# Optimization experiments

Hardware: AMD Instinct MI355X
Metric: run time of the kernel (lower is better)

Reference implementation:

```python
import jax, jax.numpy as jnp
import numpy as np
from jax import lax

N, T, IN, H, HEADS, OUT, E = 20000, 32, 32, 64, 4, 1, 320000


def setup_inputs() -> dict:
    key = jax.random.key(0)
    ks = jax.random.split(key, 18)
    s = 0.1
    inp = {
        "x": jax.random.normal(ks[0], (N, T, IN), jnp.float32),
        "edge_index": jax.random.randint(ks[1], (2, E), 0, N, dtype=jnp.int32),
        # LSTM layer 0 (PyTorch gate order i,f,g,o)
        "l0_Wih": jax.random.normal(ks[2], (4 * H, IN), jnp.float32) * s,
        "l0_Whh": jax.random.normal(ks[3], (4 * H, H), jnp.float32) * s,
        "l0_bih": jax.random.normal(ks[4], (4 * H,), jnp.float32) * s,
        "l0_bhh": jax.random.normal(ks[5], (4 * H,), jnp.float32) * s,
        # LSTM layer 1
        "l1_Wih": jax.random.normal(ks[6], (4 * H, H), jnp.float32) * s,
        "l1_Whh": jax.random.normal(ks[7], (4 * H, H), jnp.float32) * s,
        "l1_bih": jax.random.normal(ks[8], (4 * H,), jnp.float32) * s,
        "l1_bhh": jax.random.normal(ks[9], (4 * H,), jnp.float32) * s,
        # GAT layer 1: in=H, out=H, heads=HEADS (concat)
        "g1_w": jax.random.normal(ks[10], (H, HEADS * H), jnp.float32) * s,
        "g1_as": jax.random.normal(ks[11], (1, HEADS, H), jnp.float32) * s,
        "g1_ad": jax.random.normal(ks[12], (1, HEADS, H), jnp.float32) * s,
        "g1_b": jnp.zeros((HEADS * H,), jnp.float32),
        # GAT layer 2: in=HEADS*H, out=OUT, heads=1
        "g2_w": jax.random.normal(ks[13], (HEADS * H, OUT), jnp.float32) * s,
        "g2_as": jax.random.normal(ks[14], (1, 1, OUT), jnp.float32) * s,
        "g2_ad": jax.random.normal(ks[15], (1, 1, OUT), jnp.float32) * s,
        "g2_b": jnp.zeros((OUT,), jnp.float32),
    }
    return inp


def _lstm_layer(x, Wih, Whh, bih, bhh):
    # x: [N, T, F] -> [N, T, H]
    n = x.shape[0]
    h0 = jnp.zeros((n, Whh.shape[1]), x.dtype)

    def step(carry, xt):
        h, c = carry
        g = xt @ Wih.T + h @ Whh.T + bih + bhh  # [N, 4H]
        i, f, gg, o = jnp.split(g, 4, axis=-1)
        c = jax.nn.sigmoid(f) * c + jax.nn.sigmoid(i) * jnp.tanh(gg)
        h = jax.nn.sigmoid(o) * jnp.tanh(c)
        return (h, c), h

    _, hs = lax.scan(step, (h0, h0), jnp.swapaxes(x, 0, 1))
    return jnp.swapaxes(hs, 0, 1)


def _gat(x, src, dst, n, W, a_src, a_dst, b, heads, outc):
    # PyG GATConv (eval mode, add_self_loops already applied to src/dst)
    xh = (x @ W).reshape(n, heads, outc)              # [N, heads, C]
    al_s = (xh * a_src).sum(-1)                       # [N, heads]
    al_d = (xh * a_dst).sum(-1)
    e = jax.nn.leaky_relu(al_s[src] + al_d[dst], 0.2)  # [E, heads]
    m = jax.ops.segment_max(e, dst, num_segments=n)
    m = jnp.where(jnp.isfinite(m), m, 0.0)
    ex = jnp.exp(e - m[dst])
    den = jax.ops.segment_sum(ex, dst, num_segments=n)
    w = ex / (den[dst] + 1e-16)                       # segment softmax over dst
    out = jax.ops.segment_sum(xh[src] * w[..., None], dst, num_segments=n)
    return out.reshape(n, heads * outc) + b


def reference(x, edge_index, l0_Wih, l0_Whh, l0_bih, l0_bhh, l1_Wih, l1_Whh,
              l1_bih, l1_bhh, g1_w, g1_as, g1_ad, g1_b, g2_w, g2_as, g2_ad, g2_b):
    n = x.shape[0]
    loops = jnp.arange(n, dtype=edge_index.dtype)
    ei = jnp.concatenate([edge_index, jnp.stack([loops, loops])], axis=1)
    src, dst = ei[0], ei[1]
    h = _lstm_layer(x, l0_Wih, l0_Whh, l0_bih, l0_bhh)
    h = _lstm_layer(h, l1_Wih, l1_Whh, l1_bih, l1_bhh)
    h = h[:, -1, :]  # node features from last timestep
    h = jax.nn.relu(_gat(h, src, dst, n, g1_w, g1_as, g1_ad, g1_b, HEADS, H))
    return _gat(h, src, dst, n, g2_w, g2_as, g2_ad, g2_b, 1, OUT)
```

## Files before the change

### kernel.cpp

```cpp
#include <hip/hip_runtime.h>
#include <math.h>

#define NN   20000
#define TT   32
#define INF_ 32
#define HID  64
#define NH   4
#define EE   320000
#define ETOT (EE + NN)
#define ZROW 164
#define NB   80

typedef __attribute__((ext_vector_type(8))) short bf16x8;
typedef __attribute__((ext_vector_type(4))) short short4v;
typedef __attribute__((ext_vector_type(4))) float f32x4;

static __device__ __forceinline__ float lrelu(float x){ return x>0.0f ? x : 0.2f*x; }

static __device__ __forceinline__ unsigned short f2bf(float f){
  unsigned u = __float_as_uint(f);
  unsigned r = u + 0x7fffu + ((u>>16)&1u);
  return (unsigned short)(r>>16);
}
static __device__ __forceinline__ float bf2f(unsigned short h){ return __uint_as_float(((unsigned)h)<<16); }

static __device__ __forceinline__ float lstm_cell(float gi, float gf, float gg, float go, float& c){
  float ef = __expf(-gf), ei = __expf(-gi), eg = __expf(-2.0f*gg);
  float pN = c*(1.0f+ei)*(1.0f+eg) + (1.0f-eg)*(1.0f+ef);
  float pD = (1.0f+ef)*(1.0f+ei)*(1.0f+eg);
  float cc = pN * __builtin_amdgcn_rcpf(pD);
  c = cc;
  float eo = __expf(-go), ec = __expf(-2.0f*cc);
  return (1.0f-ec) * __builtin_amdgcn_rcpf((1.0f+eo)*(1.0f+ec));
}

static __device__ __forceinline__ void edge_sd(const int* __restrict__ ei, int e, int& s, int& d){
  if (e < EE){ s = ei[e]; d = ei[EE + e]; } else { s = e - EE; d = s; }
}

__global__ void kzero_int(int* __restrict__ p, int n){
  int i = blockIdx.x*256 + threadIdx.x;
  if (i < n) p[i] = 0;
}

__global__ void pack_weights(const float* __restrict__ Wih0, const float* __restrict__ Whh0,
                             const float* __restrict__ bih0, const float* __restrict__ bhh0,
                             const float* __restrict__ Wih1, const float* __restrict__ Whh1,
                             const float* __restrict__ bih1, const float* __restrict__ bhh1,
                             unsigned short* __restrict__ Wpk,
                             float* __restrict__ b0, float* __restrict__ b1){
  int idx = blockIdx.x*256 + threadIdx.x;
  if (idx < 49152){
    int fb = idx >> 9;
    int h  = fb & 1;
    int t2 = fb >> 1;
    int ks = t2 % 3, tl = t2 / 3;
    int r  = idx & 511;
    int l  = r >> 3, j = r & 7;
    int pr = l & 15;
    int g  = (pr&3)*64 + tl*4 + (pr>>2);
    int k  = ks*32 + 4*(l>>4) + (j & 3) + 16*(j >> 2);
    float src = (k < 32) ? Wih0[g*32 + k] : Whh0[g*64 + (k - 32)];
    unsigned short hi = f2bf(src);
    Wpk[idx] = h ? f2bf(src - bf2f(hi)) : hi;
  } else if (idx < 114688){
    int idx2 = idx - 49152;
    int fb = idx2 >> 9;
    int h  = fb & 1;
    int t2 = fb >> 1;
    int ks = t2 & 3, tl = t2 >> 2;
    int r  = idx2 & 511;
    int l  = r >> 3, j = r & 7;
    int pr = l & 15;
    int g  = (pr&3)*64 + tl*4 + (pr>>2);
    int k  = ks*32 + 4*(l>>4) + (j & 3) + 16*(j >> 2);
    float src = (k < 64) ? Wih1[g*64 + k] : Whh1[g*64 + (k - 64)];
    unsigned short hi = f2bf(src);
    Wpk[idx] = h ? f2bf(src - bf2f(hi)) : hi;
  } else {
    int m = idx - 114688;
    if (m < 256) b0[m] = bih0[m] + bhh0[m];
    else if (m < 512) b1[m-256] = bih1[m-256] + bhh1[m-256];
  }
}

__global__ void count_deg(const int* __restrict__ ei, int* __restrict__ deg){
  int e = blockIdx.x*256 + threadIdx.x;
  if (e >= ETOT) return;
  int s, d; edge_sd(ei, e, s, d);
  atomicAdd(deg + d, 1);
}

__global__ void scan_deg(const int* __restrict__ deg, int* __restrict__ indptr, int* __restrict__ cursor){
  __shared__ int part[256];
  const int t = threadIdx.x;
  const int CH = (NN + 255) / 256;
  const int c0 = t * CH;
  int sum = 0;
  for (int i=0;i<CH;i++){ int idx=c0+i; if (idx<NN) sum += deg[idx]; }
  part[t] = sum; __syncthreads();
  int val = sum;
  for (int off=1; off<256; off<<=1){
    int add = (t>=off) ? part[t-off] : 0;
    __syncthreads();
    val += add; part[t] = val;
    __syncthreads();
  }
  int run = val - sum;
  for (int i=0;i<CH;i++){
    int idx=c0+i;
    if (idx<NN){ indptr[idx]=run; cursor[idx]=run; run += deg[idx]; }
  }
  if (t == 0) indptr[NN] = ETOT;
}

__global__ void scatter_edges(const int* __restrict__ ei, int* __restrict__ cursor, int* __restrict__ csr_src){
  int e = blockIdx.x*256 + threadIdx.x;
  if (e >= ETOT) return;
  int s, d; edge_sd(ei, e, s, d);
  int pos = atomicAdd(cursor + d, 1);
  csr_src[pos] = s;
}

#define PIN_LOAD(dst, p) asm volatile( \
    "global_load_dwordx4 %0, %1, off\n\t" \
    "s_waitcnt vmcnt(0)" \
    : "=&v"(dst) : "v"(p))

__global__ __launch_bounds__(1024)
__attribute__((amdgpu_waves_per_eu(4, 4)))
void lstm_mfma(
    const float* __restrict__ x,
    const unsigned short* __restrict__ Wpk,
    const float* __restrict__ b0, const float* __restrict__ b1,
    float* __restrict__ h1out)
{
  __shared__ unsigned short Zh[NB*ZROW];
  __shared__ unsigned short Zl[NB*ZROW];

  const int tid  = threadIdx.x;
  const int lane = tid & 63;
  const int w    = __builtin_amdgcn_readfirstlane(tid >> 6);
  const int ln15 = lane & 15;
  const int lq   = lane >> 4;
  const int gbase = blockIdx.x * NB;

  const bf16x8* wp = (const bf16x8*)Wpk;

  bf16x8 wA0h[3], wA0l[3], wA1h[4], wA1l[4];
#pragma unroll
  for (int ks=0; ks<3; ++ks){
    PIN_LOAD(wA0h[ks], wp + ((w*3+ks)*2+0)*64 + lane);
    PIN_LOAD(wA0l[ks], wp + ((w*3+ks)*2+1)*64 + lane);
  }
#pragma unroll
  for (int ks=0; ks<4; ++ks){
    PIN_LOAD(wA1h[ks], wp + 6144 + ((w*4+ks)*2+0)*64 + lane);
    PIN_LOAD(wA1l[ks], wp + 6144 + ((w*4+ks)*2+1)*64 + lane);
  }

  f32x4 bv0, bv1;
  {
    const int u = w*4 + lq;
#pragma unroll
    for (int j=0; j<4; ++j){ bv0[j] = b0[j*64+u]; bv1[j] = b1[j*64+u]; }
  }

  const int xn = tid >> 3;
  const int xk = (tid & 7) * 4;
  const float* xp = x + (size_t)(gbase + ((xn < NB) ? xn : 0))*(TT*INF_) + xk;
  const bool xth = (tid < 640);

  for (int i = tid; i < NB*ZROW/2; i += 1024){ ((unsigned*)Zh)[i] = 0; ((unsigned*)Zl)[i] = 0; }
  __syncthreads();
  if (xth){
    float4 v = *(const float4*)xp;
    unsigned short h_[4], l_[4];
    h_[0]=f2bf(v.x); h_[1]=f2bf(v.y); h_[2]=f2bf(v.z); h_[3]=f2bf(v.w);
    l_[0]=f2bf(v.x-bf2f(h_[0])); l_[1]=f2bf(v.y-bf2f(h_[1]));
    l_[2]=f2bf(v.z-bf2f(h_[2])); l_[3]=f2bf(v.w-bf2f(h_[3]));
    *(uint2*)&Zh[xn*ZROW + xk] = make_uint2((unsigned)h_[0]|((unsigned)h_[1]<<16),(unsigned)h_[2]|((unsigned)h_[3]<<16));
    *(uint2*)&Zl[xn*ZROW + xk] = make_uint2((unsigned)l_[0]|((unsigned)l_[1]<<16),(unsigned)l_[2]|((unsigned)l_[3]<<16));
  }
  __syncthreads();

  float c0[5], c1[5];
#pragma unroll
  for (int i=0;i<5;i++){ c0[i]=0.f; c1[i]=0.f; }
  f32x4 aL1[5];

#define ZFRAG(Zb, node, kz) ({                                            \
    const unsigned short* _p = &Zb[(node)*ZROW + (kz) + 4*lq];            \
    short4v _a = *(const short4v*)_p;                                     \
    short4v _b = *(const short4v*)(_p + 16);                              \
    __builtin_shufflevector(_a, _b, 0,1,2,3,4,5,6,7); })

#define MF(acc, A, B) acc = __builtin_amdgcn_mfma_f32_16x16x32_bf16((A),(B),(acc),0,0,0)

#define HWRITE(hv, col) {                                                 \
    const unsigned short _hh = f2bf(hv);                                  \
    Zh[_n*ZROW + (col)] = _hh;                                            \
    Zl[_n*ZROW + (col)] = f2bf((hv) - bf2f(_hh)); }

  for (int t=0; t<TT; ++t){
    float4 xv;
    const bool dox = xth && (t+1 < TT);
    if (dox) xv = *(const float4*)(xp + (size_t)(t+1)*INF_);

    if (t > 0){
      const int uc = 96 + w*4 + lq;
#pragma unroll
      for (int GG=0; GG<5; ++GG){
        const int _n = GG*16 + ln15;
        float h = lstm_cell(aL1[GG][0], aL1[GG][1], aL1[GG][2], aL1[GG][3], c1[GG]);
        HWRITE(h, uc);
      }
    }

    f32x4 aL0[5];
#pragma unroll
    for (int GG=0; GG<5; ++GG) aL0[GG] = bv0;

#pragma unroll
    for (int ks=0; ks<3; ++ks){
      const int kz = ks*32;
#pragma unroll
      for (int GG=0; GG<5; ++GG){
        const bf16x8 zh = ZFRAG(Zh, GG*16+ln15, kz);
        const bf16x8 zl = ZFRAG(Zl, GG*16+ln15, kz);
        MF(aL0[GG], wA0h[ks], zh); MF(aL0[GG], wA0h[ks], zl); MF(aL0[GG], wA0l[ks], zh);
      }
    }
    __syncthreads();

    {
      const int uc = 32 + w*4 + lq;
#pragma unroll
      for (int GG=0; GG<5; ++GG){
        const int _n = GG*16 + ln15;
        float h = lstm_cell(aL0[GG][0], aL0[GG][1], aL0[GG][2], aL0[GG][3], c0[GG]);
        HWRITE(h, uc);
      }
    }
    if (dox){
      unsigned short h_[4], l_[4];
      h_[0]=f2bf(xv.x); h_[1]=f2bf(xv.y); h_[2]=f2bf(xv.z); h_[3]=f2bf(xv.w);
      l_[0]=f2bf(xv.x-bf2f(h_[0])); l_[1]=f2bf(xv.y-bf2f(h_[1]));
      l_[2]=f2bf(xv.z-bf2f(h_[2])); l_[3]=f2bf(xv.w-bf2f(h_[3]));
      *(uint2*)&Zh[xn*ZROW + xk] = make_uint2((unsigned)h_[0]|((unsigned)h_[1]<<16),(unsigned)h_[2]|((unsigned)h_[3]<<16));
      *(uint2*)&Zl[xn*ZROW + xk] = make_uint2((unsigned)l_[0]|((unsigned)l_[1]<<16),(unsigned)l_[2]|((unsigned)l_[3]<<16));
    }

#pragma unroll
    for (int GG=0; GG<5; ++GG) aL1[GG] = bv1;

#pragma unroll
    for (int ks=2; ks<4; ++ks){
      const int kz = 32 + ks*32;
#pragma unroll
      for (int GG=0; GG<5; ++GG){
        const bf16x8 zh = ZFRAG(Zh, GG*16+ln15, kz);
        const bf16x8 zl = ZFRAG(Zl, GG*16+ln15, kz);
        MF(aL1[GG], wA1h[ks], zh); MF(aL1[GG], wA1h[ks], zl); MF(aL1[GG], wA1l[ks], zh);
      }
    }
    __syncthreads();

#pragma unroll
    for (int ks=0; ks<2; ++ks){
      const int kz = 32 + ks*32;
#pragma unroll
      for (int GG=0; GG<5; ++GG){
        const bf16x8 zh = ZFRAG(Zh, GG*16+ln15, kz);
        const bf16x8 zl = ZFRAG(Zl, GG*16+ln15, kz);
        MF(aL1[GG], wA1h[ks], zh); MF(aL1[GG], wA1h[ks], zl); MF(aL1[GG], wA1l[ks], zh);
      }
    }
    __syncthreads();
  }

  {
    const int uc = 96 + w*4 + lq;
#pragma unroll
    for (int GG=0; GG<5; ++GG){
      const int _n = GG*16 + ln15;
      float h = lstm_cell(aL1[GG][0], aL1[GG][1], aL1[GG][2], aL1[GG][3], c1[GG]);
      HWRITE(h, uc);
    }
  }
  __syncthreads();

  for (int o = tid; o < NB*64; o += 1024){
    const int n = o >> 6, u = o & 63;
    h1out[(size_t)(gbase+n)*64 + u] = bf2f(Zh[n*ZROW + 96 + u]) + bf2f(Zl[n*ZROW + 96 + u]);
  }
#undef ZFRAG
#undef MF
#undef HWRITE
}

__global__ __launch_bounds__(256) void gat1_prep(const float* __restrict__ h1, const float* __restrict__ W,
  const float* __restrict__ as_, const float* __restrict__ ad_,
  float* __restrict__ xh, float* __restrict__ als, float* __restrict__ ald)
{
  __shared__ float hs[8][64];
  const int nb0 = blockIdx.x * 8;
  const int o  = threadIdx.x;
  const int q  = o >> 6, u = o & 63;
  for (int i = o; i < 512; i += 256){
    hs[i>>6][i&63] = h1[(size_t)(nb0 + (i>>6))*64 + (i&63)];
  }
  __syncthreads();
  float acc[8];
#pragma unroll
  for (int nd=0; nd<8; ++nd) acc[nd] = 0.f;
  for (int k=0; k<64; ++k){
    const float wv = W[k*256 + o];
#pragma unroll
    for (int nd=0; nd<8; ++nd) acc[nd] = fmaf(hs[nd][k], wv, acc[nd]);
  }
  const float asv = as_[o], adv = ad_[o];
#pragma unroll
  for (int nd=0; nd<8; ++nd){
    xh[(size_t)(nb0+nd)*256 + o] = acc[nd];
    float ps = acc[nd] * asv;
    float pd = acc[nd] * adv;
#pragma unroll
    for (int off=32; off>=1; off>>=1){ ps += __shfl_xor(ps, off); pd += __shfl_xor(pd, off); }
    if (u == 0){ als[(nb0+nd)*4 + q] = ps; ald[(nb0+nd)*4 + q] = pd; }
  }
}

__global__ __launch_bounds__(256) void gat1_gather(
  const int* __restrict__ indptr, const int* __restrict__ csr_src,
  const float* __restrict__ als, const float* __restrict__ ald,
  const float* __restrict__ xh,  const float* __restrict__ b1g,
  const float* __restrict__ w2,  const float* __restrict__ as2, const float* __restrict__ ad2,
  float* __restrict__ xh2, float* __restrict__ a2s, float* __restrict__ a2d)
{
  const int d = blockIdx.x*4 + (threadIdx.x >> 6);
  const int lane = threadIdx.x & 63;
  if (d >= NN) return;
  const int p0 = indptr[d], p1 = indptr[d+1];

  float aldv[4];
#pragma unroll
  for (int q=0;q<4;q++) aldv[q] = ald[d*4+q];

  float mx[4];
#pragma unroll
  for (int q=0;q<4;q++) mx[q] = -3.4e38f;
  for (int e=p0+lane; e<p1; e+=64){
    int s = csr_src[e];
#pragma unroll
    for (int q=0;q<4;q++){
      float ev = lrelu(als[s*4+q] + aldv[q]);
      mx[q] = fmaxf(mx[q], ev);
    }
  }
#pragma unroll
  for (int off=32; off>=1; off>>=1){
#pragma unroll
    for (int q=0;q<4;q++) mx[q] = fmaxf(mx[q], __shfl_xor(mx[q], off));
  }

  const int q = lane >> 4;
  const float mq = mx[q];
  const float aldq = aldv[q];
  float ax=0.f, ay=0.f, az=0.f, aw=0.f, den=0.f;
  int s_next = (p0 < p1) ? csr_src[p0] : 0;
  for (int e=p0; e<p1; ++e){
    const int s = s_next;
    if (e+1 < p1) s_next = csr_src[e+1];
    float ev = lrelu(als[s*4+q] + aldq);
    float ex = __expf(ev - mq);
    den += ex;
    float4 v = *(const float4*)(xh + (size_t)s*256 + lane*4);
    ax = fmaf(ex, v.x, ax); ay = fmaf(ex, v.y, ay);
    az = fmaf(ex, v.z, az); aw = fmaf(ex, v.w, aw);
  }
  const float rr = 1.0f/(den + 1e-16f);
  const int o = lane*4;
  float v0 = ax*rr + b1g[o+0];
  float v1 = ay*rr + b1g[o+1];
  float v2 = az*rr + b1g[o+2];
  float v3 = aw*rr + b1g[o+3];
  v0 = v0>0.f?v0:0.f; v1 = v1>0.f?v1:0.f; v2 = v2>0.f?v2:0.f; v3 = v3>0.f?v3:0.f;
  float part = v0*w2[o+0] + v1*w2[o+1] + v2*w2[o+2] + v3*w2[o+3];
#pragma unroll
  for (int off=32; off>=1; off>>=1) part += __shfl_xor(part, off);
  if (lane == 0){
    xh2[d] = part;
    a2s[d] = part * as2[0];
    a2d[d] = part * ad2[0];
  }
}

__global__ __launch_bounds__(256) void gat2_gather(
  const int* __restrict__ indptr, const int* __restrict__ csr_src,
  const float* __restrict__ a2s, const float* __restrict__ a2d,
  const float* __restrict__ xh2, const float* __restrict__ b2,
  float* __restrict__ out)
{
  const int d = blockIdx.x*4 + (threadIdx.x >> 6);
  const int lane = threadIdx.x & 63;
  if (d >= NN) return;
  const int p0 = indptr[d], p1 = indptr[d+1];
  const float add = a2d[d];

  float mx = -3.4e38f;
  for (int e=p0+lane; e<p1; e+=64){
    int s = csr_src[e];
    mx = fmaxf(mx, lrelu(a2s[s] + add));
  }
#pragma unroll
  for (int off=32; off>=1; off>>=1) mx = fmaxf(mx, __shfl_xor(mx, off));

  float den = 0.f, num = 0.f;
  for (int e=p0+lane; e<p1; e+=64){
    int s = csr_src[e];
    float ev = lrelu(a2s[s] + add);
    float ex = __expf(ev - mx);
    den += ex;
    num = fmaf(ex, xh2[s], num);
  }
#pragma unroll
  for (int off=32; off>=1; off>>=1){ den += __shfl_xor(den, off); num += __shfl_xor(num, off); }
  if (lane == 0) out[d] = num/(den + 1e-16f) + b2[0];
}

extern "C" void kernel_launch(void* const* d_in, const int* in_sizes, int n_in,
                              void* d_out, int out_size, void* d_ws, size_t ws_size,
                              hipStream_t stream)
{
  const float* x    = (const float*)d_in[0];
  const int*   ei   = (const int*)d_in[1];
  const float* Wih0 = (const float*)d_in[2];
  const float* Whh0 = (const float*)d_in[3];
  const float* bih0 = (const float*)d_in[4];
  const float* bhh0 = (const float*)d_in[5];
  const float* Wih1 = (const float*)d_in[6];
  const float* Whh1 = (const float*)d_in[7];
  const float* bih1 = (const float*)d_in[8];
  const float* bhh1 = (const float*)d_in[9];
  const float* g1w  = (const float*)d_in[10];
  const float* g1as = (const float*)d_in[11];
  const float* g1ad = (const float*)d_in[12];
  const float* g1b  = (const float*)d_in[13];
  const float* g2w  = (const float*)d_in[14];
  const float* g2as = (const float*)d_in[15];
  const float* g2ad = (const float*)d_in[16];
  const float* g2b  = (const float*)d_in[17];

  float* ws  = (float*)d_ws;
  unsigned short* Wpk = (unsigned short*)ws;
  float* b0  = ws + 57344;
  float* b1  = b0 + 256;
  float* h1  = b1 + 256;
  float* xh  = h1 + 1280000;
  float* als = xh + 5120000;
  float* ald = als + 80000;
  float* xh2 = ald + 80000;
  float* a2s = xh2 + 20000;
  float* a2d = a2s + 20000;
  int*   deg    = (int*)(a2d + 20000);
  int*   indptr = deg + 20000;
  int*   cursor = indptr + 20001;
  int*   csr    = cursor + 20000;

  kzero_int<<<(NN+255)/256, 256, 0, stream>>>(deg, NN);
  pack_weights<<<450, 256, 0, stream>>>(Wih0,Whh0,bih0,bhh0,Wih1,Whh1,bih1,bhh1,Wpk,b0,b1);
  count_deg<<<(ETOT+255)/256, 256, 0, stream>>>(ei, deg);
  scan_deg<<<1, 256, 0, stream>>>(deg, indptr, cursor);
  scatter_edges<<<(ETOT+255)/256, 256, 0, stream>>>(ei, cursor, csr);
  lstm_mfma<<<250, 1024, 0, stream>>>(x, Wpk, b0, b1, h1);
  gat1_prep<<<NN/8, 256, 0, stream>>>(h1, g1w, g1as, g1ad, xh, als, ald);
  gat1_gather<<<(NN+3)/4, 256, 0, stream>>>(indptr, csr, als, ald, xh, g1b, g2w, g2as, g2ad, xh2, a2s, a2d);
  gat2_gather<<<(NN+3)/4, 256, 0, stream>>>(indptr, csr, a2s, a2d, xh2, g2b, (float*)d_out);
}
```

Baseline: 412.9 us.

## Reschedule LSTM MFMA chunks around barriers, pack bf16 conversions, widen GAT prep tile

Reorders the fused two-layer LSTM time loop so MFMA chunks that do not depend on freshly written hidden state are interleaved with the gate nonlinearities. This removes one __syncthreads per timestep by carrying the final layer-1 chunks across the loop boundary. The fp32-to-bf16 hi/lo splitting now uses the packed v_cvt_pk_bf16_f32 instruction to cut ALU work. gat1_prep processes 16 nodes per block instead of 8 to reuse each weight load more. The barrier reordering depends on subtle LDS read/write ordering, and the larger accumulator raises register pressure.

```diff
diff --git a/kernel.cpp b/kernel.cpp
--- a/kernel.cpp
+++ b/kernel.cpp
@@ -171,16 +171,24 @@
   const float* xp = x + (size_t)(gbase + ((xn < NB) ? xn : 0))*(TT*INF_) + xk;
   const bool xth = (tid < 640);
 
+#define XSTAGE(v) {                                                       \
+    unsigned pkA, pkB, plA, plB;                                          \
+    asm("v_cvt_pk_bf16_f32 %0,%1,%2":"=v"(pkA):"v"((v).x),"v"((v).y));    \
+    asm("v_cvt_pk_bf16_f32 %0,%1,%2":"=v"(pkB):"v"((v).z),"v"((v).w));    \
+    float l0_ = (v).x - __uint_as_float(pkA<<16);                         \
+    float l1_ = (v).y - __uint_as_float(pkA & 0xffff0000u);               \
+    float l2_ = (v).z - __uint_as_float(pkB<<16);                         \
+    float l3_ = (v).w - __uint_as_float(pkB & 0xffff0000u);               \
+    asm("v_cvt_pk_bf16_f32 %0,%1,%2":"=v"(plA):"v"(l0_),"v"(l1_));        \
+    asm("v_cvt_pk_bf16_f32 %0,%1,%2":"=v"(plB):"v"(l2_),"v"(l3_));        \
+    *(uint2*)&Zh[xn*ZROW + xk] = make_uint2(pkA, pkB);                    \
+    *(uint2*)&Zl[xn*ZROW + xk] = make_uint2(plA, plB); }
+
   for (int i = tid; i < NB*ZROW/2; i += 1024){ ((unsigned*)Zh)[i] = 0; ((unsigned*)Zl)[i] = 0; }
   __syncthreads();
   if (xth){
     float4 v = *(const float4*)xp;
-    unsigned short h_[4], l_[4];
-    h_[0]=f2bf(v.x); h_[1]=f2bf(v.y); h_[2]=f2bf(v.z); h_[3]=f2bf(v.w);
-    l_[0]=f2bf(v.x-bf2f(h_[0])); l_[1]=f2bf(v.y-bf2f(h_[1]));
-    l_[2]=f2bf(v.z-bf2f(h_[2])); l_[3]=f2bf(v.w-bf2f(h_[3]));
-    *(uint2*)&Zh[xn*ZROW + xk] = make_uint2((unsigned)h_[0]|((unsigned)h_[1]<<16),(unsigned)h_[2]|((unsigned)h_[3]<<16));
-    *(uint2*)&Zl[xn*ZROW + xk] = make_uint2((unsigned)l_[0]|((unsigned)l_[1]<<16),(unsigned)l_[2]|((unsigned)l_[3]<<16));
+    XSTAGE(v);
   }
   __syncthreads();
 
@@ -197,96 +205,87 @@
 
 #define MF(acc, A, B) acc = __builtin_amdgcn_mfma_f32_16x16x32_bf16((A),(B),(acc),0,0,0)
 
-#define HWRITE(hv, col) {                                                 \
+#define WPAIR(ha, hb, GA, GB, col) {                                      \
+    unsigned pk_, pl_;                                                    \
+    asm("v_cvt_pk_bf16_f32 %0,%1,%2":"=v"(pk_):"v"(ha),"v"(hb));          \
+    float la_ = (ha) - __uint_as_float(pk_<<16);                          \
+    float lb_ = (hb) - __uint_as_float(pk_ & 0xffff0000u);                \
+    asm("v_cvt_pk_bf16_f32 %0,%1,%2":"=v"(pl_):"v"(la_),"v"(lb_));        \
+    Zh[((GA)*16+ln15)*ZROW + (col)] = (unsigned short)pk_;                \
+    Zh[((GB)*16+ln15)*ZROW + (col)] = (unsigned short)(pk_>>16);          \
+    Zl[((GA)*16+ln15)*ZROW + (col)] = (unsigned short)pl_;                \
+    Zl[((GB)*16+ln15)*ZROW + (col)] = (unsigned short)(pl_>>16); }
+
+#define WSINGLE(hv, GG, col) {                                            \
+    const int _n = (GG)*16 + ln15;                                        \
     const unsigned short _hh = f2bf(hv);                                  \
     Zh[_n*ZROW + (col)] = _hh;                                            \
     Zl[_n*ZROW + (col)] = f2bf((hv) - bf2f(_hh)); }
+
+#define CHUNK(ACCS, KZ, WH, WL)                                           \
+    _Pragma("unroll")                                                     \
+    for (int GG=0; GG<5; ++GG){                                           \
+      const bf16x8 zh = ZFRAG(Zh, GG*16+ln15, KZ);                        \
+      const bf16x8 zl = ZFRAG(Zl, GG*16+ln15, KZ);                        \
+      MF(ACCS[GG], WH, zh); MF(ACCS[GG], WH, zl); MF(ACCS[GG], WL, zh);   \
+    }
 
   for (int t=0; t<TT; ++t){
     float4 xv;
     const bool dox = xth && (t+1 < TT);
     if (dox) xv = *(const float4*)(xp + (size_t)(t+1)*INF_);
 
+    f32x4 aL0[5];
+#pragma unroll
+    for (int GG=0; GG<5; ++GG) aL0[GG] = bv0;
+
+    CHUNK(aL0, 0, wA0h[0], wA0l[0]);
+
     if (t > 0){
       const int uc = 96 + w*4 + lq;
-#pragma unroll
-      for (int GG=0; GG<5; ++GG){
-        const int _n = GG*16 + ln15;
-        float h = lstm_cell(aL1[GG][0], aL1[GG][1], aL1[GG][2], aL1[GG][3], c1[GG]);
-        HWRITE(h, uc);
-      }
+      float h0_ = lstm_cell(aL1[0][0], aL1[0][1], aL1[0][2], aL1[0][3], c1[0]);
+      float h1_ = lstm_cell(aL1[1][0], aL1[1][1], aL1[1][2], aL1[1][3], c1[1]);
+      float h2_ = lstm_cell(aL1[2][0], aL1[2][1], aL1[2][2], aL1[2][3], c1[2]);
+      float h3_ = lstm_cell(aL1[3][0], aL1[3][1], aL1[3][2], aL1[3][3], c1[3]);
+      float h4_ = lstm_cell(aL1[4][0], aL1[4][1], aL1[4][2], aL1[4][3], c1[4]);
+      WPAIR(h0_, h1_, 0, 1, uc); WPAIR(h2_, h3_, 2, 3, uc); WSINGLE(h4_, 4, uc);
     }
 
-    f32x4 aL0[5];
-#pragma unroll
-    for (int GG=0; GG<5; ++GG) aL0[GG] = bv0;
-
-#pragma unroll
-    for (int ks=0; ks<3; ++ks){
-      const int kz = ks*32;
-#pragma unroll
-      for (int GG=0; GG<5; ++GG){
-        const bf16x8 zh = ZFRAG(Zh, GG*16+ln15, kz);
-        const bf16x8 zl = ZFRAG(Zl, GG*16+ln15, kz);
-        MF(aL0[GG], wA0h[ks], zh); MF(aL0[GG], wA0h[ks], zl); MF(aL0[GG], wA0l[ks], zh);
-      }
-    }
+    CHUNK(aL0, 32, wA0h[1], wA0l[1]);
+    CHUNK(aL0, 64, wA0h[2], wA0l[2]);
     __syncthreads();
+
+#pragma unroll
+    for (int GG=0; GG<5; ++GG) aL1[GG] = bv1;
+
+    CHUNK(aL1, 96, wA1h[2], wA1l[2]);
 
     {
       const int uc = 32 + w*4 + lq;
-#pragma unroll
-      for (int GG=0; GG<5; ++GG){
-        const int _n = GG*16 + ln15;
-        float h = lstm_cell(aL0[GG][0], aL0[GG][1], aL0[GG][2], aL0[GG][3], c0[GG]);
-        HWRITE(h, uc);
-      }
+      float h0_ = lstm_cell(aL0[0][0], aL0[0][1], aL0[0][2], aL0[0][3], c0[0]);
+      float h1_ = lstm_cell(aL0[1][0], aL0[1][1], aL0[1][2], aL0[1][3], c0[1]);
+      float h2_ = lstm_cell(aL0[2][0], aL0[2][1], aL0[2][2], aL0[2][3], c0[2]);
+      float h3_ = lstm_cell(aL0[3][0], aL0[3][1], aL0[3][2], aL0[3][3], c0[3]);
+      float h4_ = lstm_cell(aL0[4][0], aL0[4][1], aL0[4][2], aL0[4][3], c0[4]);
+      WPAIR(h0_, h1_, 0, 1, uc); WPAIR(h2_, h3_, 2, 3, uc); WSINGLE(h4_, 4, uc);
     }
-    if (dox){
-      unsigned short h_[4], l_[4];
-      h_[0]=f2bf(xv.x); h_[1]=f2bf(xv.y); h_[2]=f2bf(xv.z); h_[3]=f2bf(xv.w);
-      l_[0]=f2bf(xv.x-bf2f(h_[0])); l_[1]=f2bf(xv.y-bf2f(h_[1]));
-      l_[2]=f2bf(xv.z-bf2f(h_[2])); l_[3]=f2bf(xv.w-bf2f(h_[3]));
-      *(uint2*)&Zh[xn*ZROW + xk] = make_uint2((unsigned)h_[0]|((unsigned)h_[1]<<16),(unsigned)h_[2]|((unsigned)h_[3]<<16));
-      *(uint2*)&Zl[xn*ZROW + xk] = make_uint2((unsigned)l_[0]|((unsigned)l_[1]<<16),(unsigned)l_[2]|((unsigned)l_[3]<<16));
-    }
-
-#pragma unroll
-    for (int GG=0; GG<5; ++GG) aL1[GG] = bv1;
-
-#pragma unroll
-    for (int ks=2; ks<4; ++ks){
-      const int kz = 32 + ks*32;
-#pragma unroll
-      for (int GG=0; GG<5; ++GG){
-        const bf16x8 zh = ZFRAG(Zh, GG*16+ln15, kz);
-        const bf16x8 zl = ZFRAG(Zl, GG*16+ln15, kz);
-        MF(aL1[GG], wA1h[ks], zh); MF(aL1[GG], wA1h[ks], zl); MF(aL1[GG], wA1l[ks], zh);
-      }
-    }
+    if (dox) XSTAGE(xv);
+
+    CHUNK(aL1, 128, wA1h[3], wA1l[3]);
     __syncthreads();
 
-#pragma unroll
-    for (int ks=0; ks<2; ++ks){
-      const int kz = 32 + ks*32;
-#pragma unroll
-      for (int GG=0; GG<5; ++GG){
-        const bf16x8 zh = ZFRAG(Zh, GG*16+ln15, kz);
-        const bf16x8 zl = ZFRAG(Zl, GG*16+ln15, kz);
-        MF(aL1[GG], wA1h[ks], zh); MF(aL1[GG], wA1h[ks], zl); MF(aL1[GG], wA1l[ks], zh);
-      }
-    }
-    __syncthreads();
+    CHUNK(aL1, 32, wA1h[0], wA1l[0]);
+    CHUNK(aL1, 64, wA1h[1], wA1l[1]);
   }
 
   {
     const int uc = 96 + w*4 + lq;
-#pragma unroll
-    for (int GG=0; GG<5; ++GG){
-      const int _n = GG*16 + ln15;
-      float h = lstm_cell(aL1[GG][0], aL1[GG][1], aL1[GG][2], aL1[GG][3], c1[GG]);
-      HWRITE(h, uc);
-    }
+    float h0_ = lstm_cell(aL1[0][0], aL1[0][1], aL1[0][2], aL1[0][3], c1[0]);
+    float h1_ = lstm_cell(aL1[1][0], aL1[1][1], aL1[1][2], aL1[1][3], c1[1]);
+    float h2_ = lstm_cell(aL1[2][0], aL1[2][1], aL1[2][2], aL1[2][3], c1[2]);
+    float h3_ = lstm_cell(aL1[3][0], aL1[3][1], aL1[3][2], aL1[3][3], c1[3]);
+    float h4_ = lstm_cell(aL1[4][0], aL1[4][1], aL1[4][2], aL1[4][3], c1[4]);
+    WPAIR(h0_, h1_, 0, 1, uc); WPAIR(h2_, h3_, 2, 3, uc); WSINGLE(h4_, 4, uc);
   }
   __syncthreads();
 
@@ -296,32 +295,35 @@
   }
 #undef ZFRAG
 #undef MF
-#undef HWRITE
+#undef WPAIR
+#undef WSINGLE
+#undef CHUNK
+#undef XSTAGE
 }
 
 __global__ __launch_bounds__(256) void gat1_prep(const float* __restrict__ h1, const float* __restrict__ W,
   const float* __restrict__ as_, const float* __restrict__ ad_,
   float* __restrict__ xh, float* __restrict__ als, float* __restrict__ ald)
 {
-  __shared__ float hs[8][64];
-  const int nb0 = blockIdx.x * 8;
+  __shared__ float hs[16][64];
+  const int nb0 = blockIdx.x * 16;
   const int o  = threadIdx.x;
   const int q  = o >> 6, u = o & 63;
-  for (int i = o; i < 512; i += 256){
+  for (int i = o; i < 1024; i += 256){
     hs[i>>6][i&63] = h1[(size_t)(nb0 + (i>>6))*64 + (i&63)];
   }
   __syncthreads();
-  float acc[8];
-#pragma unroll
-  for (int nd=0; nd<8; ++nd) acc[nd] = 0.f;
+  float acc[16];
+#pragma unroll
+  for (int nd=0; nd<16; ++nd) acc[nd] = 0.f;
   for (int k=0; k<64; ++k){
     const float wv = W[k*256 + o];
 #pragma unroll
-    for (int nd=0; nd<8; ++nd) acc[nd] = fmaf(hs[nd][k], wv, acc[nd]);
+    for (int nd=0; nd<16; ++nd) acc[nd] = fmaf(hs[nd][k], wv, acc[nd]);
   }
   const float asv = as_[o], adv = ad_[o];
 #pragma unroll
-  for (int nd=0; nd<8; ++nd){
+  for (int nd=0; nd<16; ++nd){
     xh[(size_t)(nb0+nd)*256 + o] = acc[nd];
     float ps = acc[nd] * asv;
     float pd = acc[nd] * adv;
@@ -474,7 +476,7 @@
   scan_deg<<<1, 256, 0, stream>>>(deg, indptr, cursor);
   scatter_edges<<<(ETOT+255)/256, 256, 0, stream>>>(ei, cursor, csr);
   lstm_mfma<<<250, 1024, 0, stream>>>(x, Wpk, b0, b1, h1);
-  gat1_prep<<<NN/8, 256, 0, stream>>>(h1, g1w, g1as, g1ad, xh, als, ald);
+  gat1_prep<<<NN/16, 256, 0, stream>>>(h1, g1w, g1as, g1ad, xh, als, ald);
   gat1_gather<<<(NN+3)/4, 256, 0, stream>>>(indptr, csr, als, ald, xh, g1b, g2w, g2as, g2ad, xh2, a2s, a2d);
   gat2_gather<<<(NN+3)/4, 256, 0, stream>>>(indptr, csr, a2s, a2d, xh2, g2b, (float*)d_out);
 }
```

New measurement: 405.7 us. No clear change (-1.7%).
